# Kernel tuning notes

Hardware: AMD Instinct MI355X
Metric: run time of the kernel (lower is better)

Reference implementation:

```python
import math
import jax, jax.numpy as jnp
import numpy as np

E = 1024   # embed_dim
H = 16     # num_heads
DH = E // H
EPS = 1e-8

def round_ste(x):
    # straight-through round (matches brevitas STE behavior)
    return x + jax.lax.stop_gradient(jnp.round(x) - x)

def _scale(x, qmax):
    # dynamic per-tensor abs-max scale (stand-in for brevitas calibrated scale)
    return jnp.maximum(jnp.max(jnp.abs(x)) / qmax, EPS)

def fq(x, s, qmin, qmax):
    # fake-quantize: quantize to int grid, dequantize back to float
    return jnp.clip(round_ste(x / s), qmin, qmax) * s

def quant_linear(x, W, b):
    # Int8ActPerTensorFloat input, Int8WeightPerTensorFloat (narrow range) weight, Int32Bias
    s_x = _scale(x, 128.0)
    s_w = _scale(W, 127.0)
    xq = fq(x, s_x, -128, 127)
    wq = fq(W, s_w, -127, 127)
    y = xq @ wq.T
    if b is not None:
        s_b = s_x * s_w
        y = y + round_ste(b / s_b) * s_b
    return y

def setup_inputs() -> dict:
    k = jax.random.key(0)
    ks = jax.random.split(k, 7)
    S, B = 1024, 4
    return {
        "query": jax.random.normal(ks[0], (S, B, E), jnp.float32),
        "key": jax.random.normal(ks[1], (S, B, E), jnp.float32),
        "value": jax.random.normal(ks[2], (S, B, E), jnp.float32),
        "in_proj_weight": jax.random.normal(ks[3], (3 * E, E), jnp.float32) * 0.02,
        "in_proj_bias": jax.random.normal(ks[4], (3 * E,), jnp.float32) * 0.02,
        "out_proj_weight": jax.random.normal(ks[5], (E, E), jnp.float32) * 0.02,
        "out_proj_bias": jax.random.normal(ks[6], (E,), jnp.float32) * 0.02,
    }

def reference(query, key, value, in_proj_weight, in_proj_bias, out_proj_weight, out_proj_bias):
    S, B, _ = query.shape
    Wq, Wk, Wv = jnp.split(in_proj_weight, 3, axis=0)
    bq, bk, bv = jnp.split(in_proj_bias, 3)
    # quantized QKV projections (packed in_proj split per-input)
    q = quant_linear(query, Wq, bq)   # (S,B,E)
    k = quant_linear(key, Wk, bk)
    v = quant_linear(value, Wv, bv)

    def to_heads(x):  # (S,B,E) -> (B*H, S, DH)
        return x.reshape(S, B * H, DH).transpose(1, 0, 2)

    q = to_heads(q)
    k = to_heads(k)
    v = to_heads(v)

    # q_scaled quant (int8)
    q = q / math.sqrt(DH)
    q = fq(q, _scale(q, 128.0), -128, 127)
    # k_transposed quant (int8)
    kt = k.transpose(0, 2, 1)  # (B*H, DH, S)
    kt = fq(kt, _scale(kt, 128.0), -128, 127)

    attn = q @ kt                      # (B*H, S, S); softmax_input_quant=None -> identity
    attn = jax.nn.softmax(attn, axis=-1)
    # attn_output_weights quant (uint8)
    s_a = jnp.maximum(jnp.max(attn) / 255.0, EPS)
    attn = jnp.clip(round_ste(attn / s_a), 0, 255) * s_a
    # v quant (int8)
    v = fq(v, _scale(v, 128.0), -128, 127)

    out = attn @ v                     # (B*H, S, DH)
    out = out.transpose(1, 0, 2).reshape(S, B, E)
    out = quant_linear(out, out_proj_weight, out_proj_bias)
    return out
```

## Files before the change

### kernel.cpp

```cpp
#include <hip/hip_runtime.h>
#include <stdint.h>

typedef unsigned short u16;
typedef __attribute__((ext_vector_type(8))) short bf16x8;
typedef __attribute__((ext_vector_type(4))) float f32x4;

#define S_LEN 1024
#define BATCH 4
#define EMB   1024
#define NH    16
#define DHEAD 64
#define BHEAD 64
#define NTOK  4096
#define KDIM  1024
#define NDIM  1024
#define EPSF  1e-8f
#define LOG2E 1.4426950408889634f

#define MFMA16(a,b,c) __builtin_amdgcn_mfma_f32_16x16x32_bf16((a),(b),(c),0,0,0)

#define GLOAD16(g, l) __builtin_amdgcn_global_load_lds( \
    (const __attribute__((address_space(1))) void*)(g), \
    (__attribute__((address_space(3))) void*)(l), 16, 0, 0)

#define EXP2F(x) __builtin_amdgcn_exp2f(x)

__device__ __forceinline__ u16 f2bf(float f){
  return (u16)(__float_as_uint(f) >> 16);
}

__device__ __forceinline__ float wave_max(float v){
#pragma unroll
  for (int off = 32; off > 0; off >>= 1) v = fmaxf(v, __shfl_xor(v, off));
  return v;
}


__global__ void k_zero(float* sc){
  if (threadIdx.x < 16) sc[threadIdx.x] = 0.0f;
}

struct AQDesc { const float* x; u16* y; int n4; int slot; float qdiv; float lo; };
struct AQTable { AQDesc d[7]; };

__global__ __launch_bounds__(256) void k_absmax7(AQTable t, int* __restrict__ sci){
  const int bid = blockIdx.x;
  int seg, b0, nb;
  if (bid < 1536){ seg = bid >> 9; b0 = seg << 9; nb = 512; }
  else { seg = 3 + ((bid - 1536) >> 7); b0 = 1536 + ((seg - 3) << 7); nb = 128; }
  const AQDesc D = t.d[seg];
  float m = 0.0f;
  const float4* x4 = (const float4*)D.x;
  for (int i = (bid - b0)*256 + threadIdx.x; i < D.n4; i += nb*256){
    float4 v = x4[i];
    m = fmaxf(m, fmaxf(fmaxf(fabsf(v.x), fabsf(v.y)), fmaxf(fabsf(v.z), fabsf(v.w))));
  }
  m = wave_max(m);
  __shared__ float red[4];
  int lane = threadIdx.x & 63, w = threadIdx.x >> 6;
  if (lane == 0) red[w] = m;
  __syncthreads();
  if (threadIdx.x == 0){
    float mm = fmaxf(fmaxf(red[0], red[1]), fmaxf(red[2], red[3]));
    atomicMax(sci + D.slot, __float_as_int(mm));
  }
}

__global__ __launch_bounds__(256) void k_quant7(AQTable t, const float* __restrict__ sc){
  const int bid = blockIdx.x;
  int seg, b0, nb;
  if (bid < 1536){ seg = bid >> 9; b0 = seg << 9; nb = 512; }
  else { seg = 3 + ((bid - 1536) >> 7); b0 = 1536 + ((seg - 3) << 7); nb = 128; }
  const AQDesc D = t.d[seg];
  const float s = fmaxf(sc[D.slot] / D.qdiv, EPSF);
  const float lo = D.lo;
  const float4* x4 = (const float4*)D.x;
  for (int i = (bid - b0)*256 + threadIdx.x; i < D.n4; i += nb*256){
    float4 v = x4[i];
    union { u16 o[4]; uint2 u; } ou;
    float tt;
    tt = fminf(fmaxf(rintf(v.x / s), lo), 127.f); ou.o[0] = f2bf(tt);
    tt = fminf(fmaxf(rintf(v.y / s), lo), 127.f); ou.o[1] = f2bf(tt);
    tt = fminf(fmaxf(rintf(v.z / s), lo), 127.f); ou.o[2] = f2bf(tt);
    tt = fminf(fmaxf(rintf(v.w / s), lo), 127.f); ou.o[3] = f2bf(tt);
    ((uint2*)D.y)[i] = ou.u;
  }
}

__global__ __launch_bounds__(256) void k_quant(const float* __restrict__ x,
    u16* __restrict__ y, int n4, const float* __restrict__ sc, int slot){
  const float s = fmaxf(sc[slot] / 128.0f, EPSF);
  const float4* x4 = (const float4*)x;
  for (int i = blockIdx.x*256 + threadIdx.x; i < n4; i += gridDim.x*256){
    float4 v = x4[i];
    union { u16 o[4]; uint2 u; } ou;
    float tt;
    tt = fminf(fmaxf(rintf(v.x / s), -128.f), 127.f); ou.o[0] = f2bf(tt);
    tt = fminf(fmaxf(rintf(v.y / s), -128.f), 127.f); ou.o[1] = f2bf(tt);
    tt = fminf(fmaxf(rintf(v.z / s), -128.f), 127.f); ou.o[2] = f2bf(tt);
    tt = fminf(fmaxf(rintf(v.w / s), -128.f), 127.f); ou.o[3] = f2bf(tt);
    ((uint2*)y)[i] = ou.u;
  }
}

__device__ __forceinline__ void gemm_body(const u16* __restrict__ A,
    const u16* __restrict__ W, const float* __restrict__ bias,
    float* __restrict__ out, float s_b, int rowBase, int colBase,
    int* __restrict__ amax_out, u16 (*As)[32], u16 (*Bs)[32], float* red){
  const int tid = threadIdx.x;
  const int wid = tid >> 6, lane = tid & 63;
  const int wm = wid >> 2, wn = wid & 3;
  const int rr = lane & 15, kk = (lane >> 4) * 8;
  const int sr = tid >> 2, scb = (tid & 3) * 8;
  const u16* Arow = &A[(size_t)(rowBase + sr)*KDIM + scb];
  const u16* Wrow = &W[(size_t)(colBase + sr)*KDIM + scb];
  f32x4 c[4][2] = {};
  for (int k0 = 0; k0 < KDIM; k0 += 32){
    __syncthreads();
    GLOAD16(Arow + k0, &As[wid*16][0]);
    GLOAD16(Wrow + k0, &Bs[wid*16][0]);
    __syncthreads();
    bf16x8 af[4], bfr[2];
#pragma unroll
    for (int i = 0; i < 4; i++) af[i] = *(const bf16x8*)&As[wm*64 + i*16 + rr][kk];
#pragma unroll
    for (int j = 0; j < 2; j++) bfr[j] = *(const bf16x8*)&Bs[wn*32 + j*16 + rr][kk];
#pragma unroll
    for (int i = 0; i < 4; i++)
#pragma unroll
      for (int j = 0; j < 2; j++)
        c[i][j] = MFMA16(af[i], bfr[j], c[i][j]);
  }
  float lmax = 0.0f;
  const int r0 = (lane >> 4) * 4, ccol = lane & 15;
#pragma unroll
  for (int j = 0; j < 2; j++){
    int col = colBase + wn*32 + j*16 + ccol;
    float rb = rintf(bias[col] / s_b);
#pragma unroll
    for (int i = 0; i < 4; i++){
      int rowb = rowBase + wm*64 + i*16 + r0;
#pragma unroll
      for (int rI = 0; rI < 4; rI++){
        float y = s_b * (c[i][j][rI] + rb);
        out[(size_t)(rowb + rI)*NDIM + col] = y;
        lmax = fmaxf(lmax, fabsf(y));
      }
    }
  }
  lmax = wave_max(lmax);
  if (lane == 0) red[wid] = lmax;
  __syncthreads();
  if (tid == 0){
    float mm = red[0];
#pragma unroll
    for (int i2 = 1; i2 < 8; i2++) mm = fmaxf(mm, red[i2]);
    atomicMax(amax_out, __float_as_int(mm));
  }
}

__global__ __launch_bounds__(512) void k_gemm3(const u16* __restrict__ Xall,
    const u16* __restrict__ Wall, const float* __restrict__ ball,
    float* __restrict__ Yall, const float* __restrict__ sc, int* __restrict__ sci){
  __shared__ u16 As[128][32];
  __shared__ u16 Bs[128][32];
  __shared__ float red[8];
  const int orig = blockIdx.x;
  const int xcd = orig & 7, sl = orig >> 3;
  const int seg = sl >> 5;
  const int t2 = xcd*32 + (sl & 31);
  const int by = t2 >> 3, bx = t2 & 7;
  const float s_x = fmaxf(sc[seg] / 128.0f, EPSF);
  const float s_w = fmaxf(sc[3 + seg] / 127.0f, EPSF);
  gemm_body(Xall + (size_t)seg*NTOK*KDIM, Wall + (size_t)seg*KDIM*NDIM,
            ball + seg*1024, Yall + (size_t)seg*NTOK*NDIM, s_x*s_w,
            by*128, bx*128, sci + 7 + seg, As, Bs, red);
}

__global__ __launch_bounds__(512) void k_gemm1(const u16* __restrict__ A,
    const u16* __restrict__ W, const float* __restrict__ bias,
    float* __restrict__ out, const float* __restrict__ sc,
    int sx_slot, int sw_slot, int* __restrict__ amax_out){
  __shared__ u16 As[128][32];
  __shared__ u16 Bs[128][32];
  __shared__ float red[8];
  const int orig = blockIdx.x;
  const int t2 = (orig & 7)*32 + (orig >> 3);
  const int by = t2 >> 3, bx = t2 & 7;
  const float s_x = fmaxf(sc[sx_slot] / 128.0f, EPSF);
  const float s_w = fmaxf(sc[sw_slot] / 127.0f, EPSF);
  gemm_body(A, W, bias, out, s_x*s_w, by*128, bx*128, amax_out, As, Bs, red);
}

__global__ __launch_bounds__(256) void k_quant_heads(const float* __restrict__ qf,
    const float* __restrict__ kf, const float* __restrict__ vf,
    u16* __restrict__ qh, u16* __restrict__ kh, u16* __restrict__ vt,
    const float* __restrict__ sc){
  const float s_q = fmaxf((sc[7]*0.125f)/128.0f, EPSF);
  const float s_k = fmaxf(sc[8]/128.0f, EPSF);
  const float s_v = fmaxf(sc[9]/128.0f, EPSF);
  __shared__ u16 tile[64][80];
  const int bx = blockIdx.x;
  const int st = bx & 15, hh = (bx >> 4) & 15, b = bx >> 8;
  const int t = threadIdx.x;
  const int sl = t >> 2, dc = (t & 3) * 16;
  const size_t row = (size_t)(st*64 + sl)*BATCH + b;
  const size_t ibase = row*EMB + hh*DHEAD + dc;
  const int bh = b*NH + hh;
  float vq[16], vk[16], vv[16];
#pragma unroll
  for (int i = 0; i < 4; i++){
    *(float4*)&vq[i*4] = *(const float4*)&qf[ibase + i*4];
    *(float4*)&vk[i*4] = *(const float4*)&kf[ibase + i*4];
    *(float4*)&vv[i*4] = *(const float4*)&vf[ibase + i*4];
  }
  alignas(16) u16 oq[16], ok[16];
#pragma unroll
  for (int i = 0; i < 16; i++){
    float tq = fminf(fmaxf(rintf((vq[i]*0.125f)/s_q), -128.f), 127.f);
    float tk = fminf(fmaxf(rintf(vk[i]/s_k), -128.f), 127.f);
    float tv = fminf(fmaxf(rintf(vv[i]/s_v), -128.f), 127.f);
    oq[i] = f2bf(tq); ok[i] = f2bf(tk);
    tile[dc + i][sl] = f2bf(tv);
  }
  const size_t qoff = ((size_t)bh*S_LEN + st*64 + sl)*DHEAD + dc;
  *(bf16x8*)&qh[qoff]     = *(const bf16x8*)&oq[0];
  *(bf16x8*)&qh[qoff + 8] = *(const bf16x8*)&oq[8];
  *(bf16x8*)&kh[qoff]     = *(const bf16x8*)&ok[0];
  *(bf16x8*)&kh[qoff + 8] = *(const bf16x8*)&ok[8];
  __syncthreads();
  const int d = t >> 2, sc4 = (t & 3) * 16;
  alignas(16) u16 ov[16];
#pragma unroll
  for (int i = 0; i < 16; i++) ov[i] = tile[d][sc4 + i];
  const size_t voff = ((size_t)bh*DHEAD + d)*S_LEN + st*64 + sc4;
  *(bf16x8*)&vt[voff]     = *(const bf16x8*)&ov[0];
  *(bf16x8*)&vt[voff + 8] = *(const bf16x8*)&ov[8];
}

__global__ __launch_bounds__(256) void k_attn1(const u16* __restrict__ qh,
    const u16* __restrict__ kh, float* __restrict__ mrow, float* __restrict__ lrow,
    const float* __restrict__ sc, int* __restrict__ sci){
  __shared__ u16 Ks[64][64];
  __shared__ float red2[4];
  const int orig = blockIdx.x;
  const int tile = (orig & 7) * 128 + (orig >> 3);
  const int bhead = tile >> 4, q0 = (tile & 15) * 64;
  const int tid = threadIdx.x, w = tid >> 6, lane = tid & 63;
  const int rr = lane & 15, g = lane >> 4, kk = g * 8;
  const int lr3 = lane >> 3, lc = lane & 7;
  const float s_q = fmaxf((sc[7]*0.125f)/128.0f, EPSF);
  const float s_k = fmaxf(sc[8]/128.0f, EPSF);
  const float s_qk = s_q * s_k;
  const u16* qbase = qh + ((size_t)bhead*S_LEN + q0 + w*16)*DHEAD;
  const u16* kbase = kh + (size_t)bhead*S_LEN*DHEAD;
  bf16x8 a0 = *(const bf16x8*)&qbase[rr*DHEAD + kk];
  bf16x8 a1 = *(const bf16x8*)&qbase[rr*DHEAD + 32 + kk];
  float m[4] = {-1e30f, -1e30f, -1e30f, -1e30f};
  float l[4] = {0.f, 0.f, 0.f, 0.f};
  for (int cch = 0; cch < 16; cch++){
    const int n0 = cch * 64;
    __syncthreads();
#pragma unroll
    for (int i = 0; i < 2; i++){
      int r = w*16 + i*8 + lr3;
      GLOAD16(&kbase[(size_t)(n0 + r)*DHEAD + ((lc ^ (r & 7)) << 3)], &Ks[w*16 + i*8][0]);
    }
    __syncthreads();
    float sv[4][4];
#pragma unroll
    for (int nt = 0; nt < 4; nt++){
      int row = nt*16 + rr;
      bf16x8 b0 = *(const bf16x8*)((const u16*)Ks + row*64 + (((g    ) ^ (row & 7)) << 3));
      bf16x8 b1 = *(const bf16x8*)((const u16*)Ks + row*64 + (((4 + g) ^ (row & 7)) << 3));
      f32x4 acc = {};
      acc = MFMA16(a0, b0, acc);
      acc = MFMA16(a1, b1, acc);
#pragma unroll
      for (int r = 0; r < 4; r++) sv[nt][r] = acc[r]*s_qk;
    }
#pragma unroll
    for (int r = 0; r < 4; r++){
      float cm = fmaxf(fmaxf(sv[0][r], sv[1][r]), fmaxf(sv[2][r], sv[3][r]));
      float mn = fmaxf(m[r], cm);
      l[r] *= EXP2F((m[r] - mn)*LOG2E);
      m[r] = mn;
#pragma unroll
      for (int nt = 0; nt < 4; nt++)
        l[r] += EXP2F((sv[nt][r] - m[r])*LOG2E);
    }
  }
#pragma unroll
  for (int off = 1; off < 16; off <<= 1){
#pragma unroll
    for (int r = 0; r < 4; r++){
      float mo = __shfl_xor(m[r], off), lo = __shfl_xor(l[r], off);
      float mn = fmaxf(m[r], mo);
      l[r] = l[r]*EXP2F((m[r] - mn)*LOG2E) + lo*EXP2F((mo - mn)*LOG2E);
      m[r] = mn;
    }
  }
  if (rr == 0){
    int rowb = q0 + w*16 + g*4;
#pragma unroll
    for (int r = 0; r < 4; r++){
      mrow[(size_t)bhead*S_LEN + rowb + r] = m[r];
      lrow[(size_t)bhead*S_LEN + rowb + r] = l[r];
    }
  }
  float im = 0.0f;
#pragma unroll
  for (int r = 0; r < 4; r++) im = fmaxf(im, 1.0f / l[r]);
  im = wave_max(im);
  if (lane == 0) red2[w] = im;
  __syncthreads();
  if (tid == 0){
    float mm = fmaxf(fmaxf(red2[0], red2[1]), fmaxf(red2[2], red2[3]));
    atomicMax(sci + 13, __float_as_int(mm));
  }
}

__global__ void k_sa_final(float* sc, const int* sci){
  if (threadIdx.x == 0)
    sc[11] = fmaxf(__int_as_float(sci[13]) / 255.0f, EPSF);
}

__global__ __launch_bounds__(256) void k_attn2(const u16* __restrict__ qh,
    const u16* __restrict__ kh, const u16* __restrict__ vt,
    const float* __restrict__ mrow, const float* __restrict__ lrow,
    float* __restrict__ aout, const float* __restrict__ sc, int* __restrict__ amax_out){
  __shared__ u16 Ks[64][64];
  __shared__ u16 Vs[64][64];
  __shared__ u16 P[4][16][72];
  __shared__ float red[4];
  const int orig = blockIdx.x;
  const int tile = (orig & 7) * 128 + (orig >> 3);
  const int bhead = tile >> 4, q0 = (tile & 15) * 64;
  const int tid = threadIdx.x, w = tid >> 6, lane = tid & 63;
  const int rr = lane & 15, g = lane >> 4, kk = g * 8;
  const int lr3 = lane >> 3, lc = lane & 7;
  const float s_q = fmaxf((sc[7]*0.125f)/128.0f, EPSF);
  const float s_k = fmaxf(sc[8]/128.0f, EPSF);
  const float s_qk = s_q * s_k;
  const float s_v = fmaxf(sc[9]/128.0f, EPSF);
  const float s_a = sc[11];
  const float fac = s_a * s_v;
  const u16* qbase = qh + ((size_t)bhead*S_LEN + q0 + w*16)*DHEAD;
  const u16* kbase = kh + (size_t)bhead*S_LEN*DHEAD;
  const u16* vbase = vt + (size_t)bhead*DHEAD*S_LEN;
  bf16x8 a0 = *(const bf16x8*)&qbase[rr*DHEAD + kk];
  bf16x8 a1 = *(const bf16x8*)&qbase[rr*DHEAD + 32 + kk];
  float mr[4], inv[4];
  {
    int rowb = q0 + w*16 + g*4;
#pragma unroll
    for (int r = 0; r < 4; r++){
      mr[r]  = mrow[(size_t)bhead*S_LEN + rowb + r];
      inv[r] = 1.0f / (lrow[(size_t)bhead*S_LEN + rowb + r] * s_a);
    }
  }
  f32x4 cpv[4] = {};
  for (int cch = 0; cch < 16; cch++){
    const int n0 = cch * 64;
    __syncthreads();
#pragma unroll
    for (int i = 0; i < 2; i++){
      int r = w*16 + i*8 + lr3;
      GLOAD16(&kbase[(size_t)(n0 + r)*DHEAD + ((lc ^ (r & 7)) << 3)], &Ks[w*16 + i*8][0]);
      int d = w*16 + i*8 + lr3;
      GLOAD16(&vbase[(size_t)d*S_LEN + n0 + ((lc ^ (d & 7)) << 3)], &Vs[w*16 + i*8][0]);
    }
    __syncthreads();
#pragma unroll
    for (int nt = 0; nt < 4; nt++){
      int row = nt*16 + rr;
      bf16x8 b0 = *(const bf16x8*)((const u16*)Ks + row*64 + (((g    ) ^ (row & 7)) << 3));
      bf16x8 b1 = *(const bf16x8*)((const u16*)Ks + row*64 + (((4 + g) ^ (row & 7)) << 3));
      f32x4 acc = {};
      acc = MFMA16(a0, b0, acc);
      acc = MFMA16(a1, b1, acc);
#pragma unroll
      for (int r = 0; r < 4; r++){
        float e  = EXP2F((acc[r]*s_qk - mr[r])*LOG2E);
        float pq = fminf(rintf(e * inv[r]), 255.0f);
        P[w][g*4 + r][nt*16 + rr] = f2bf(pq);
      }
    }
    bf16x8 pa0 = *(const bf16x8*)&P[w][rr][kk];
    bf16x8 pa1 = *(const bf16x8*)&P[w][rr][32 + kk];
#pragma unroll
    for (int f = 0; f < 4; f++){
      int row = f*16 + rr;
      bf16x8 v0 = *(const bf16x8*)((const u16*)Vs + row*64 + (((g    ) ^ (row & 7)) << 3));
      bf16x8 v1 = *(const bf16x8*)((const u16*)Vs + row*64 + (((4 + g) ^ (row & 7)) << 3));
      cpv[f] = MFMA16(pa0, v0, cpv[f]);
      cpv[f] = MFMA16(pa1, v1, cpv[f]);
    }
  }
  const int b = bhead >> 4, hh = bhead & 15;
  float lmax = 0.0f;
#pragma unroll
  for (int f = 0; f < 4; f++){
    int d = f*16 + rr;
#pragma unroll
    for (int r = 0; r < 4; r++){
      int srow = q0 + w*16 + g*4 + r;
      float y = fac * cpv[f][r];
      aout[(size_t)(srow*BATCH + b)*EMB + hh*DHEAD + d] = y;
      lmax = fmaxf(lmax, fabsf(y));
    }
  }
  lmax = wave_max(lmax);
  __syncthreads();
  if (lane == 0) red[w] = lmax;
  __syncthreads();
  if (tid == 0){
    float mm = fmaxf(fmaxf(red[0], red[1]), fmaxf(red[2], red[3]));
    atomicMax(amax_out, __float_as_int(mm));
  }
}

extern "C" void kernel_launch(void* const* d_in, const int* in_sizes, int n_in,
                              void* d_out, int out_size, void* d_ws, size_t ws_size,
                              hipStream_t stream){
  const float* query = (const float*)d_in[0];
  const float* key   = (const float*)d_in[1];
  const float* value = (const float*)d_in[2];
  const float* inW   = (const float*)d_in[3];
  const float* inB   = (const float*)d_in[4];
  const float* outW  = (const float*)d_in[5];
  const float* outB  = (const float*)d_in[6];
  float* out = (float*)d_out;

  char* ws = (char*)d_ws;
  float* sc  = (float*)ws;
  int*   sci = (int*)ws;
  u16* WQQ = (u16*)(ws + 256);
  u16* WKQ = WQQ + 1024*1024;
  u16* WVQ = WKQ + 1024*1024;
  u16* WOQ = WVQ + 1024*1024;
  u16* XQ  = WOQ + 1024*1024;
  u16* XK  = XQ + NTOK*1024;
  u16* XV  = XK + NTOK*1024;
  float* QF = (float*)(XV + NTOK*1024);
  float* KF = QF + NTOK*1024;
  float* VF = KF + NTOK*1024;
  float* MROW = VF + NTOK*1024;
  float* LROW = MROW + BHEAD*S_LEN;
  u16* QH = XQ;  u16* KH = XK;  u16* VT = XV;
  float* AOUT = QF;
  u16* AOQ = (u16*)KF;

  AQTable tab;
  tab.d[0] = { query,             XQ,  NTOK*1024/4, 0, 128.f, -128.f };
  tab.d[1] = { key,               XK,  NTOK*1024/4, 1, 128.f, -128.f };
  tab.d[2] = { value,             XV,  NTOK*1024/4, 2, 128.f, -128.f };
  tab.d[3] = { inW,               WQQ, 1024*1024/4, 3, 127.f, -127.f };
  tab.d[4] = { inW + 1024*1024,   WKQ, 1024*1024/4, 4, 127.f, -127.f };
  tab.d[5] = { inW + 2*1024*1024, WVQ, 1024*1024/4, 5, 127.f, -127.f };
  tab.d[6] = { outW,              WOQ, 1024*1024/4, 6, 127.f, -127.f };

  k_zero<<<1, 64, 0, stream>>>(sc);
  k_absmax7<<<2048, 256, 0, stream>>>(tab, sci);
  k_quant7<<<2048, 256, 0, stream>>>(tab, sc);
  k_gemm3<<<768, 512, 0, stream>>>(XQ, WQQ, inB, QF, sc, sci);
  k_quant_heads<<<1024, 256, 0, stream>>>(QF, KF, VF, QH, KH, VT, sc);
  k_attn1<<<1024, 256, 0, stream>>>(QH, KH, MROW, LROW, sc, sci);
  k_sa_final<<<1, 64, 0, stream>>>(sc, sci);
  k_attn2<<<1024, 256, 0, stream>>>(QH, KH, VT, MROW, LROW, AOUT, sc, sci + 10);
  k_quant<<<1024, 256, 0, stream>>>(AOUT, AOQ, NTOK*1024/4, sc, 10);
  k_gemm1<<<256, 512, 0, stream>>>(AOQ, WOQ, outB, out, sc, 10, 6, sci + 12);
}
```

Measured before the change: 215.0 us.

## Double-buffer LDS tiles in GEMM and attention kernels, swizzle, drop sa_final

Adds double-buffered LDS tiles to the GEMM and both attention kernels. The load of the next K-step or chunk is issued before the current one is consumed, and one barrier per iteration replaces two. It also XOR-swizzles the GEMM A/B tiles and the P scratch buffer to cut LDS bank conflicts. It removes the separate k_sa_final launch by computing s_a inside k_attn2, and replaces block reductions with per-wave atomics. The cost is double the LDS use and more atomics, which may lower occupancy.

```diff
diff --git a/kernel.cpp b/kernel.cpp
--- a/kernel.cpp
+++ b/kernel.cpp
@@ -106,30 +106,48 @@
 __device__ __forceinline__ void gemm_body(const u16* __restrict__ A,
     const u16* __restrict__ W, const float* __restrict__ bias,
     float* __restrict__ out, float s_b, int rowBase, int colBase,
-    int* __restrict__ amax_out, u16 (*As)[32], u16 (*Bs)[32], float* red){
+    int* __restrict__ amax_out, u16 (*As)[128][32], u16 (*Bs)[128][32], float* red){
   const int tid = threadIdx.x;
   const int wid = tid >> 6, lane = tid & 63;
   const int wm = wid >> 2, wn = wid & 3;
-  const int rr = lane & 15, kk = (lane >> 4) * 8;
-  const int sr = tid >> 2, scb = (tid & 3) * 8;
-  const u16* Arow = &A[(size_t)(rowBase + sr)*KDIM + scb];
-  const u16* Wrow = &W[(size_t)(colBase + sr)*KDIM + scb];
+  const int rr = lane & 15, g = lane >> 4, kk = g * 8;
+  const int sr = tid >> 2, sc4 = tid & 3;
+  const int scol = (sc4 ^ ((sr >> 1) & 3)) * 8;
+  const u16* Arow = &A[(size_t)(rowBase + sr)*KDIM + scol];
+  const u16* Wrow = &W[(size_t)(colBase + sr)*KDIM + scol];
   f32x4 c[4][2] = {};
+  int aoff[4], boff[2];
+#pragma unroll
+  for (int i = 0; i < 4; i++){
+    int row = wm*64 + i*16 + rr;
+    aoff[i] = row*32 + ((g ^ ((row >> 1) & 3)) << 3);
+  }
+#pragma unroll
+  for (int j = 0; j < 2; j++){
+    int row = wn*32 + j*16 + rr;
+    boff[j] = row*32 + ((g ^ ((row >> 1) & 3)) << 3);
+  }
+  GLOAD16(Arow, &As[0][sr][sc4*8]);
+  GLOAD16(Wrow, &Bs[0][sr][sc4*8]);
+  __syncthreads();
+  int cur = 0;
   for (int k0 = 0; k0 < KDIM; k0 += 32){
-    __syncthreads();
-    GLOAD16(Arow + k0, &As[wid*16][0]);
-    GLOAD16(Wrow + k0, &Bs[wid*16][0]);
-    __syncthreads();
+    if (k0 + 32 < KDIM){
+      GLOAD16(Arow + k0 + 32, &As[cur^1][sr][sc4*8]);
+      GLOAD16(Wrow + k0 + 32, &Bs[cur^1][sr][sc4*8]);
+    }
     bf16x8 af[4], bfr[2];
 #pragma unroll
-    for (int i = 0; i < 4; i++) af[i] = *(const bf16x8*)&As[wm*64 + i*16 + rr][kk];
-#pragma unroll
-    for (int j = 0; j < 2; j++) bfr[j] = *(const bf16x8*)&Bs[wn*32 + j*16 + rr][kk];
+    for (int i = 0; i < 4; i++) af[i]  = *(const bf16x8*)((const u16*)As[cur] + aoff[i]);
+#pragma unroll
+    for (int j = 0; j < 2; j++) bfr[j] = *(const bf16x8*)((const u16*)Bs[cur] + boff[j]);
 #pragma unroll
     for (int i = 0; i < 4; i++)
 #pragma unroll
       for (int j = 0; j < 2; j++)
         c[i][j] = MFMA16(af[i], bfr[j], c[i][j]);
+    __syncthreads();
+    cur ^= 1;
   }
   float lmax = 0.0f;
   const int r0 = (lane >> 4) * 4, ccol = lane & 15;
@@ -162,8 +180,8 @@
 __global__ __launch_bounds__(512) void k_gemm3(const u16* __restrict__ Xall,
     const u16* __restrict__ Wall, const float* __restrict__ ball,
     float* __restrict__ Yall, const float* __restrict__ sc, int* __restrict__ sci){
-  __shared__ u16 As[128][32];
-  __shared__ u16 Bs[128][32];
+  __shared__ u16 As[2][128][32];
+  __shared__ u16 Bs[2][128][32];
   __shared__ float red[8];
   const int orig = blockIdx.x;
   const int xcd = orig & 7, sl = orig >> 3;
@@ -181,8 +199,8 @@
     const u16* __restrict__ W, const float* __restrict__ bias,
     float* __restrict__ out, const float* __restrict__ sc,
     int sx_slot, int sw_slot, int* __restrict__ amax_out){
-  __shared__ u16 As[128][32];
-  __shared__ u16 Bs[128][32];
+  __shared__ u16 As[2][128][32];
+  __shared__ u16 Bs[2][128][32];
   __shared__ float red[8];
   const int orig = blockIdx.x;
   const int t2 = (orig & 7)*32 + (orig >> 3);
@@ -241,8 +259,7 @@
 __global__ __launch_bounds__(256) void k_attn1(const u16* __restrict__ qh,
     const u16* __restrict__ kh, float* __restrict__ mrow, float* __restrict__ lrow,
     const float* __restrict__ sc, int* __restrict__ sci){
-  __shared__ u16 Ks[64][64];
-  __shared__ float red2[4];
+  __shared__ u16 Ks[2][64][64];
   const int orig = blockIdx.x;
   const int tile = (orig & 7) * 128 + (orig >> 3);
   const int bhead = tile >> 4, q0 = (tile & 15) * 64;
@@ -256,23 +273,26 @@
   const u16* kbase = kh + (size_t)bhead*S_LEN*DHEAD;
   bf16x8 a0 = *(const bf16x8*)&qbase[rr*DHEAD + kk];
   bf16x8 a1 = *(const bf16x8*)&qbase[rr*DHEAD + 32 + kk];
+  const int sr0 = w*16 + lr3, sr1 = w*16 + 8 + lr3;
+  const int sco0 = (lc ^ (sr0 & 7)) << 3, sco1 = (lc ^ (sr1 & 7)) << 3;
+  GLOAD16(&kbase[(size_t)sr0*DHEAD + sco0], &Ks[0][w*16][0]);
+  GLOAD16(&kbase[(size_t)sr1*DHEAD + sco1], &Ks[0][w*16 + 8][0]);
+  __syncthreads();
+  int cur = 0;
   float m[4] = {-1e30f, -1e30f, -1e30f, -1e30f};
   float l[4] = {0.f, 0.f, 0.f, 0.f};
   for (int cch = 0; cch < 16; cch++){
-    const int n0 = cch * 64;
-    __syncthreads();
-#pragma unroll
-    for (int i = 0; i < 2; i++){
-      int r = w*16 + i*8 + lr3;
-      GLOAD16(&kbase[(size_t)(n0 + r)*DHEAD + ((lc ^ (r & 7)) << 3)], &Ks[w*16 + i*8][0]);
-    }
-    __syncthreads();
+    if (cch < 15){
+      const int n0 = (cch + 1) * 64;
+      GLOAD16(&kbase[(size_t)(n0 + sr0)*DHEAD + sco0], &Ks[cur^1][w*16][0]);
+      GLOAD16(&kbase[(size_t)(n0 + sr1)*DHEAD + sco1], &Ks[cur^1][w*16 + 8][0]);
+    }
     float sv[4][4];
 #pragma unroll
     for (int nt = 0; nt < 4; nt++){
       int row = nt*16 + rr;
-      bf16x8 b0 = *(const bf16x8*)((const u16*)Ks + row*64 + (((g    ) ^ (row & 7)) << 3));
-      bf16x8 b1 = *(const bf16x8*)((const u16*)Ks + row*64 + (((4 + g) ^ (row & 7)) << 3));
+      bf16x8 b0 = *(const bf16x8*)((const u16*)Ks[cur] + row*64 + (((g    ) ^ (row & 7)) << 3));
+      bf16x8 b1 = *(const bf16x8*)((const u16*)Ks[cur] + row*64 + (((4 + g) ^ (row & 7)) << 3));
       f32x4 acc = {};
       acc = MFMA16(a0, b0, acc);
       acc = MFMA16(a1, b1, acc);
@@ -289,6 +309,8 @@
       for (int nt = 0; nt < 4; nt++)
         l[r] += EXP2F((sv[nt][r] - m[r])*LOG2E);
     }
+    __syncthreads();
+    cur ^= 1;
   }
 #pragma unroll
   for (int off = 1; off < 16; off <<= 1){
@@ -312,27 +334,17 @@
 #pragma unroll
   for (int r = 0; r < 4; r++) im = fmaxf(im, 1.0f / l[r]);
   im = wave_max(im);
-  if (lane == 0) red2[w] = im;
-  __syncthreads();
-  if (tid == 0){
-    float mm = fmaxf(fmaxf(red2[0], red2[1]), fmaxf(red2[2], red2[3]));
-    atomicMax(sci + 13, __float_as_int(mm));
-  }
-}
-
-__global__ void k_sa_final(float* sc, const int* sci){
-  if (threadIdx.x == 0)
-    sc[11] = fmaxf(__int_as_float(sci[13]) / 255.0f, EPSF);
+  if (lane == 0) atomicMax(sci + 13, __float_as_int(im));
 }
 
 __global__ __launch_bounds__(256) void k_attn2(const u16* __restrict__ qh,
     const u16* __restrict__ kh, const u16* __restrict__ vt,
     const float* __restrict__ mrow, const float* __restrict__ lrow,
-    float* __restrict__ aout, const float* __restrict__ sc, int* __restrict__ amax_out){
-  __shared__ u16 Ks[64][64];
-  __shared__ u16 Vs[64][64];
-  __shared__ u16 P[4][16][72];
-  __shared__ float red[4];
+    float* __restrict__ aout, const float* __restrict__ sc,
+    const int* __restrict__ sci, int* __restrict__ amax_out){
+  __shared__ u16 Ks[2][64][64];
+  __shared__ u16 Vs[2][64][64];
+  __shared__ u16 P[4][16][64];
   const int orig = blockIdx.x;
   const int tile = (orig & 7) * 128 + (orig >> 3);
   const int bhead = tile >> 4, q0 = (tile & 15) * 64;
@@ -343,7 +355,7 @@
   const float s_k = fmaxf(sc[8]/128.0f, EPSF);
   const float s_qk = s_q * s_k;
   const float s_v = fmaxf(sc[9]/128.0f, EPSF);
-  const float s_a = sc[11];
+  const float s_a = fmaxf(__int_as_float(sci[13]) / 255.0f, EPSF);
   const float fac = s_a * s_v;
   const u16* qbase = qh + ((size_t)bhead*S_LEN + q0 + w*16)*DHEAD;
   const u16* kbase = kh + (size_t)bhead*S_LEN*DHEAD;
@@ -359,23 +371,30 @@
       inv[r] = 1.0f / (lrow[(size_t)bhead*S_LEN + rowb + r] * s_a);
     }
   }
+  const int sr0 = w*16 + lr3, sr1 = w*16 + 8 + lr3;
+  const int sco0 = (lc ^ (sr0 & 7)) << 3, sco1 = (lc ^ (sr1 & 7)) << 3;
+  GLOAD16(&kbase[(size_t)sr0*DHEAD + sco0], &Ks[0][w*16][0]);
+  GLOAD16(&kbase[(size_t)sr1*DHEAD + sco1], &Ks[0][w*16 + 8][0]);
+  GLOAD16(&vbase[(size_t)sr0*S_LEN + sco0], &Vs[0][w*16][0]);
+  GLOAD16(&vbase[(size_t)sr1*S_LEN + sco1], &Vs[0][w*16 + 8][0]);
+  __syncthreads();
+  int cur = 0;
   f32x4 cpv[4] = {};
+  const int poff0 = rr*64 + (((g    ) ^ (rr & 7)) << 3);
+  const int poff1 = rr*64 + (((4 + g) ^ (rr & 7)) << 3);
   for (int cch = 0; cch < 16; cch++){
-    const int n0 = cch * 64;
-    __syncthreads();
-#pragma unroll
-    for (int i = 0; i < 2; i++){
-      int r = w*16 + i*8 + lr3;
-      GLOAD16(&kbase[(size_t)(n0 + r)*DHEAD + ((lc ^ (r & 7)) << 3)], &Ks[w*16 + i*8][0]);
-      int d = w*16 + i*8 + lr3;
-      GLOAD16(&vbase[(size_t)d*S_LEN + n0 + ((lc ^ (d & 7)) << 3)], &Vs[w*16 + i*8][0]);
-    }
-    __syncthreads();
+    if (cch < 15){
+      const int n0 = (cch + 1) * 64;
+      GLOAD16(&kbase[(size_t)(n0 + sr0)*DHEAD + sco0], &Ks[cur^1][w*16][0]);
+      GLOAD16(&kbase[(size_t)(n0 + sr1)*DHEAD + sco1], &Ks[cur^1][w*16 + 8][0]);
+      GLOAD16(&vbase[(size_t)sr0*S_LEN + n0 + sco0], &Vs[cur^1][w*16][0]);
+      GLOAD16(&vbase[(size_t)sr1*S_LEN + n0 + sco1], &Vs[cur^1][w*16 + 8][0]);
+    }
 #pragma unroll
     for (int nt = 0; nt < 4; nt++){
       int row = nt*16 + rr;
-      bf16x8 b0 = *(const bf16x8*)((const u16*)Ks + row*64 + (((g    ) ^ (row & 7)) << 3));
-      bf16x8 b1 = *(const bf16x8*)((const u16*)Ks + row*64 + (((4 + g) ^ (row & 7)) << 3));
+      bf16x8 b0 = *(const bf16x8*)((const u16*)Ks[cur] + row*64 + (((g    ) ^ (row & 7)) << 3));
+      bf16x8 b1 = *(const bf16x8*)((const u16*)Ks[cur] + row*64 + (((4 + g) ^ (row & 7)) << 3));
       f32x4 acc = {};
       acc = MFMA16(a0, b0, acc);
       acc = MFMA16(a1, b1, acc);
@@ -383,19 +402,24 @@
       for (int r = 0; r < 4; r++){
         float e  = EXP2F((acc[r]*s_qk - mr[r])*LOG2E);
         float pq = fminf(rintf(e * inv[r]), 255.0f);
-        P[w][g*4 + r][nt*16 + rr] = f2bf(pq);
+        int prow = g*4 + r;
+        int pcol = nt*16 + rr;
+        int pch  = ((pcol >> 3) ^ (prow & 7)) << 3;
+        P[w][prow][pch | (pcol & 7)] = f2bf(pq);
       }
     }
-    bf16x8 pa0 = *(const bf16x8*)&P[w][rr][kk];
-    bf16x8 pa1 = *(const bf16x8*)&P[w][rr][32 + kk];
+    bf16x8 pa0 = *(const bf16x8*)((const u16*)P[w] + poff0);
+    bf16x8 pa1 = *(const bf16x8*)((const u16*)P[w] + poff1);
 #pragma unroll
     for (int f = 0; f < 4; f++){
       int row = f*16 + rr;
-      bf16x8 v0 = *(const bf16x8*)((const u16*)Vs + row*64 + (((g    ) ^ (row & 7)) << 3));
-      bf16x8 v1 = *(const bf16x8*)((const u16*)Vs + row*64 + (((4 + g) ^ (row & 7)) << 3));
+      bf16x8 v0 = *(const bf16x8*)((const u16*)Vs[cur] + row*64 + (((g    ) ^ (row & 7)) << 3));
+      bf16x8 v1 = *(const bf16x8*)((const u16*)Vs[cur] + row*64 + (((4 + g) ^ (row & 7)) << 3));
       cpv[f] = MFMA16(pa0, v0, cpv[f]);
       cpv[f] = MFMA16(pa1, v1, cpv[f]);
     }
+    __syncthreads();
+    cur ^= 1;
   }
   const int b = bhead >> 4, hh = bhead & 15;
   float lmax = 0.0f;
@@ -411,13 +435,7 @@
     }
   }
   lmax = wave_max(lmax);
-  __syncthreads();
-  if (lane == 0) red[w] = lmax;
-  __syncthreads();
-  if (tid == 0){
-    float mm = fmaxf(fmaxf(red[0], red[1]), fmaxf(red[2], red[3]));
-    atomicMax(amax_out, __float_as_int(mm));
-  }
+  if (lane == 0) atomicMax(amax_out, __float_as_int(lmax));
 }
 
 extern "C" void kernel_launch(void* const* d_in, const int* in_sizes, int n_in,
@@ -466,8 +484,7 @@
   k_gemm3<<<768, 512, 0, stream>>>(XQ, WQQ, inB, QF, sc, sci);
   k_quant_heads<<<1024, 256, 0, stream>>>(QF, KF, VF, QH, KH, VT, sc);
   k_attn1<<<1024, 256, 0, stream>>>(QH, KH, MROW, LROW, sc, sci);
-  k_sa_final<<<1, 64, 0, stream>>>(sc, sci);
-  k_attn2<<<1024, 256, 0, stream>>>(QH, KH, VT, MROW, LROW, AOUT, sc, sci + 10);
+  k_attn2<<<1024, 256, 0, stream>>>(QH, KH, VT, MROW, LROW, AOUT, sc, sci, sci + 10);
   k_quant<<<1024, 256, 0, stream>>>(AOUT, AOQ, NTOK*1024/4, sc, 10);
   k_gemm1<<<256, 512, 0, stream>>>(AOQ, WOQ, outB, out, sc, 10, 6, sci + 12);
 }
```

New measurement: 288.0 us. 1.34x slower.

## Double attention query tile per block, swizzle GEMM LDS, drop scale-finalize kernel

Applied to the files above, without the earlier changes.

The attention kernels now use 512-thread blocks covering 128 query rows, so each K/V chunk loaded into LDS is reused by twice as many waves and half as many blocks are launched. Per-wave atomics replace the block-level LDS reduction, and the separate one-thread kernel that finalized the attention scale is removed; attn2 computes that scale inline. The GEMM body applies an XOR swizzle to its LDS tile layout to avoid bank conflicts on fragment reads. In exchange, more atomics hit global memory and fewer blocks are available for latency hiding.

```diff
diff --git a/kernel.cpp b/kernel.cpp
--- a/kernel.cpp
+++ b/kernel.cpp
@@ -110,11 +110,23 @@
   const int tid = threadIdx.x;
   const int wid = tid >> 6, lane = tid & 63;
   const int wm = wid >> 2, wn = wid & 3;
-  const int rr = lane & 15, kk = (lane >> 4) * 8;
-  const int sr = tid >> 2, scb = (tid & 3) * 8;
-  const u16* Arow = &A[(size_t)(rowBase + sr)*KDIM + scb];
-  const u16* Wrow = &W[(size_t)(colBase + sr)*KDIM + scb];
+  const int rr = lane & 15, g = lane >> 4, kk = g * 8;
+  const int sr = tid >> 2, sc4 = tid & 3;
+  const int scol = (sc4 ^ ((sr >> 1) & 3)) * 8;
+  const u16* Arow = &A[(size_t)(rowBase + sr)*KDIM + scol];
+  const u16* Wrow = &W[(size_t)(colBase + sr)*KDIM + scol];
   f32x4 c[4][2] = {};
+  int aoff[4], boff[2];
+#pragma unroll
+  for (int i = 0; i < 4; i++){
+    int row = wm*64 + i*16 + rr;
+    aoff[i] = row*32 + ((g ^ ((row >> 1) & 3)) << 3);
+  }
+#pragma unroll
+  for (int j = 0; j < 2; j++){
+    int row = wn*32 + j*16 + rr;
+    boff[j] = row*32 + ((g ^ ((row >> 1) & 3)) << 3);
+  }
   for (int k0 = 0; k0 < KDIM; k0 += 32){
     __syncthreads();
     GLOAD16(Arow + k0, &As[wid*16][0]);
@@ -122,9 +134,9 @@
     __syncthreads();
     bf16x8 af[4], bfr[2];
 #pragma unroll
-    for (int i = 0; i < 4; i++) af[i] = *(const bf16x8*)&As[wm*64 + i*16 + rr][kk];
-#pragma unroll
-    for (int j = 0; j < 2; j++) bfr[j] = *(const bf16x8*)&Bs[wn*32 + j*16 + rr][kk];
+    for (int i = 0; i < 4; i++) af[i]  = *(const bf16x8*)((const u16*)As + aoff[i]);
+#pragma unroll
+    for (int j = 0; j < 2; j++) bfr[j] = *(const bf16x8*)((const u16*)Bs + boff[j]);
 #pragma unroll
     for (int i = 0; i < 4; i++)
 #pragma unroll
@@ -238,17 +250,15 @@
   *(bf16x8*)&vt[voff + 8] = *(const bf16x8*)&ov[8];
 }
 
-__global__ __launch_bounds__(256) void k_attn1(const u16* __restrict__ qh,
+__global__ __launch_bounds__(512) void k_attn1(const u16* __restrict__ qh,
     const u16* __restrict__ kh, float* __restrict__ mrow, float* __restrict__ lrow,
     const float* __restrict__ sc, int* __restrict__ sci){
   __shared__ u16 Ks[64][64];
-  __shared__ float red2[4];
   const int orig = blockIdx.x;
-  const int tile = (orig & 7) * 128 + (orig >> 3);
-  const int bhead = tile >> 4, q0 = (tile & 15) * 64;
+  const int tile = (orig & 7) * 64 + (orig >> 3);
+  const int bhead = tile >> 3, q0 = (tile & 7) * 128;
   const int tid = threadIdx.x, w = tid >> 6, lane = tid & 63;
   const int rr = lane & 15, g = lane >> 4, kk = g * 8;
-  const int lr3 = lane >> 3, lc = lane & 7;
   const float s_q = fmaxf((sc[7]*0.125f)/128.0f, EPSF);
   const float s_k = fmaxf(sc[8]/128.0f, EPSF);
   const float s_qk = s_q * s_k;
@@ -256,16 +266,14 @@
   const u16* kbase = kh + (size_t)bhead*S_LEN*DHEAD;
   bf16x8 a0 = *(const bf16x8*)&qbase[rr*DHEAD + kk];
   bf16x8 a1 = *(const bf16x8*)&qbase[rr*DHEAD + 32 + kk];
+  const int rowc = w*8 + (lane >> 3);
+  const int scol = ((lane & 7) ^ (rowc & 7)) << 3;
   float m[4] = {-1e30f, -1e30f, -1e30f, -1e30f};
   float l[4] = {0.f, 0.f, 0.f, 0.f};
   for (int cch = 0; cch < 16; cch++){
     const int n0 = cch * 64;
     __syncthreads();
-#pragma unroll
-    for (int i = 0; i < 2; i++){
-      int r = w*16 + i*8 + lr3;
-      GLOAD16(&kbase[(size_t)(n0 + r)*DHEAD + ((lc ^ (r & 7)) << 3)], &Ks[w*16 + i*8][0]);
-    }
+    GLOAD16(&kbase[(size_t)(n0 + rowc)*DHEAD + scol], &Ks[w*8][0]);
     __syncthreads();
     float sv[4][4];
 #pragma unroll
@@ -312,38 +320,27 @@
 #pragma unroll
   for (int r = 0; r < 4; r++) im = fmaxf(im, 1.0f / l[r]);
   im = wave_max(im);
-  if (lane == 0) red2[w] = im;
-  __syncthreads();
-  if (tid == 0){
-    float mm = fmaxf(fmaxf(red2[0], red2[1]), fmaxf(red2[2], red2[3]));
-    atomicMax(sci + 13, __float_as_int(mm));
-  }
-}
-
-__global__ void k_sa_final(float* sc, const int* sci){
-  if (threadIdx.x == 0)
-    sc[11] = fmaxf(__int_as_float(sci[13]) / 255.0f, EPSF);
-}
-
-__global__ __launch_bounds__(256) void k_attn2(const u16* __restrict__ qh,
+  if (lane == 0) atomicMax(sci + 13, __float_as_int(im));
+}
+
+__global__ __launch_bounds__(512) void k_attn2(const u16* __restrict__ qh,
     const u16* __restrict__ kh, const u16* __restrict__ vt,
     const float* __restrict__ mrow, const float* __restrict__ lrow,
-    float* __restrict__ aout, const float* __restrict__ sc, int* __restrict__ amax_out){
+    float* __restrict__ aout, const float* __restrict__ sc,
+    const int* __restrict__ sci, int* __restrict__ amax_out){
   __shared__ u16 Ks[64][64];
   __shared__ u16 Vs[64][64];
-  __shared__ u16 P[4][16][72];
-  __shared__ float red[4];
+  __shared__ u16 P[8][16][72];
   const int orig = blockIdx.x;
-  const int tile = (orig & 7) * 128 + (orig >> 3);
-  const int bhead = tile >> 4, q0 = (tile & 15) * 64;
+  const int tile = (orig & 7) * 64 + (orig >> 3);
+  const int bhead = tile >> 3, q0 = (tile & 7) * 128;
   const int tid = threadIdx.x, w = tid >> 6, lane = tid & 63;
   const int rr = lane & 15, g = lane >> 4, kk = g * 8;
-  const int lr3 = lane >> 3, lc = lane & 7;
   const float s_q = fmaxf((sc[7]*0.125f)/128.0f, EPSF);
   const float s_k = fmaxf(sc[8]/128.0f, EPSF);
   const float s_qk = s_q * s_k;
   const float s_v = fmaxf(sc[9]/128.0f, EPSF);
-  const float s_a = sc[11];
+  const float s_a = fmaxf(__int_as_float(sci[13]) / 255.0f, EPSF);
   const float fac = s_a * s_v;
   const u16* qbase = qh + ((size_t)bhead*S_LEN + q0 + w*16)*DHEAD;
   const u16* kbase = kh + (size_t)bhead*S_LEN*DHEAD;
@@ -359,17 +356,14 @@
       inv[r] = 1.0f / (lrow[(size_t)bhead*S_LEN + rowb + r] * s_a);
     }
   }
+  const int rowc = w*8 + (lane >> 3);
+  const int scol = ((lane & 7) ^ (rowc & 7)) << 3;
   f32x4 cpv[4] = {};
   for (int cch = 0; cch < 16; cch++){
     const int n0 = cch * 64;
     __syncthreads();
-#pragma unroll
-    for (int i = 0; i < 2; i++){
-      int r = w*16 + i*8 + lr3;
-      GLOAD16(&kbase[(size_t)(n0 + r)*DHEAD + ((lc ^ (r & 7)) << 3)], &Ks[w*16 + i*8][0]);
-      int d = w*16 + i*8 + lr3;
-      GLOAD16(&vbase[(size_t)d*S_LEN + n0 + ((lc ^ (d & 7)) << 3)], &Vs[w*16 + i*8][0]);
-    }
+    GLOAD16(&kbase[(size_t)(n0 + rowc)*DHEAD + scol], &Ks[w*8][0]);
+    GLOAD16(&vbase[(size_t)rowc*S_LEN + n0 + scol], &Vs[w*8][0]);
     __syncthreads();
 #pragma unroll
     for (int nt = 0; nt < 4; nt++){
@@ -411,13 +405,7 @@
     }
   }
   lmax = wave_max(lmax);
-  __syncthreads();
-  if (lane == 0) red[w] = lmax;
-  __syncthreads();
-  if (tid == 0){
-    float mm = fmaxf(fmaxf(red[0], red[1]), fmaxf(red[2], red[3]));
-    atomicMax(amax_out, __float_as_int(mm));
-  }
+  if (lane == 0) atomicMax(amax_out, __float_as_int(lmax));
 }
 
 extern "C" void kernel_launch(void* const* d_in, const int* in_sizes, int n_in,
@@ -465,9 +453,8 @@
   k_quant7<<<2048, 256, 0, stream>>>(tab, sc);
   k_gemm3<<<768, 512, 0, stream>>>(XQ, WQQ, inB, QF, sc, sci);
   k_quant_heads<<<1024, 256, 0, stream>>>(QF, KF, VF, QH, KH, VT, sc);
-  k_attn1<<<1024, 256, 0, stream>>>(QH, KH, MROW, LROW, sc, sci);
-  k_sa_final<<<1, 64, 0, stream>>>(sc, sci);
-  k_attn2<<<1024, 256, 0, stream>>>(QH, KH, VT, MROW, LROW, AOUT, sc, sci + 10);
+  k_attn1<<<512, 512, 0, stream>>>(QH, KH, MROW, LROW, sc, sci);
+  k_attn2<<<512, 512, 0, stream>>>(QH, KH, VT, MROW, LROW, AOUT, sc, sci, sci + 10);
   k_quant<<<1024, 256, 0, stream>>>(AOUT, AOQ, NTOK*1024/4, sc, 10);
   k_gemm1<<<256, 512, 0, stream>>>(AOQ, WOQ, outB, out, sc, 10, 6, sci + 12);
 }
```

Measured after the change: 282.9 us. 31.6% more time.

## Double GEMM K-tile to 64 with XOR-swizzled LDS, drop sa_final launch

Applied to the files above, without the earlier changes.

The shared GEMM body now stages 64-wide K slices per iteration instead of 32, which halves the number of barrier pairs per K loop. LDS rows are XOR-swizzled so the 128-byte rows do not cause bank conflicts on fragment reads. The separate single-thread kernel that computed the attention-weight scale is removed, and k_attn2 derives that scale itself from the integer amax. k_attn2's block reduction is also replaced by a per-wave atomicMax, which removes two barriers at the cost of more atomics.

```diff
diff --git a/kernel.cpp b/kernel.cpp
--- a/kernel.cpp
+++ b/kernel.cpp
@@ -106,30 +106,53 @@
 __device__ __forceinline__ void gemm_body(const u16* __restrict__ A,
     const u16* __restrict__ W, const float* __restrict__ bias,
     float* __restrict__ out, float s_b, int rowBase, int colBase,
-    int* __restrict__ amax_out, u16 (*As)[32], u16 (*Bs)[32], float* red){
+    int* __restrict__ amax_out, u16 (*As)[64], u16 (*Bs)[64], float* red){
   const int tid = threadIdx.x;
   const int wid = tid >> 6, lane = tid & 63;
   const int wm = wid >> 2, wn = wid & 3;
-  const int rr = lane & 15, kk = (lane >> 4) * 8;
-  const int sr = tid >> 2, scb = (tid & 3) * 8;
-  const u16* Arow = &A[(size_t)(rowBase + sr)*KDIM + scb];
-  const u16* Wrow = &W[(size_t)(colBase + sr)*KDIM + scb];
+  const int rr = lane & 15, g = lane >> 4;
+  const int srow = wid*8 + (lane >> 3);
+  const int sco  = ((lane & 7) ^ (lane >> 3)) << 3;
+  const u16* Arow0 = &A[(size_t)(rowBase + srow)*KDIM + sco];
+  const u16* Arow1 = &A[(size_t)(rowBase + 64 + srow)*KDIM + sco];
+  const u16* Wrow0 = &W[(size_t)(colBase + srow)*KDIM + sco];
+  const u16* Wrow1 = &W[(size_t)(colBase + 64 + srow)*KDIM + sco];
   f32x4 c[4][2] = {};
-  for (int k0 = 0; k0 < KDIM; k0 += 32){
-    __syncthreads();
-    GLOAD16(Arow + k0, &As[wid*16][0]);
-    GLOAD16(Wrow + k0, &Bs[wid*16][0]);
-    __syncthreads();
-    bf16x8 af[4], bfr[2];
-#pragma unroll
-    for (int i = 0; i < 4; i++) af[i] = *(const bf16x8*)&As[wm*64 + i*16 + rr][kk];
-#pragma unroll
-    for (int j = 0; j < 2; j++) bfr[j] = *(const bf16x8*)&Bs[wn*32 + j*16 + rr][kk];
-#pragma unroll
-    for (int i = 0; i < 4; i++)
-#pragma unroll
-      for (int j = 0; j < 2; j++)
-        c[i][j] = MFMA16(af[i], bfr[j], c[i][j]);
+  int aoff[4][2], boff[2][2];
+#pragma unroll
+  for (int i = 0; i < 4; i++){
+    int row = wm*64 + i*16 + rr;
+#pragma unroll
+    for (int h = 0; h < 2; h++)
+      aoff[i][h] = row*64 + (((h*4 + g) ^ (row & 7)) << 3);
+  }
+#pragma unroll
+  for (int j = 0; j < 2; j++){
+    int row = wn*32 + j*16 + rr;
+#pragma unroll
+    for (int h = 0; h < 2; h++)
+      boff[j][h] = row*64 + (((h*4 + g) ^ (row & 7)) << 3);
+  }
+  for (int k0 = 0; k0 < KDIM; k0 += 64){
+    __syncthreads();
+    GLOAD16(Arow0 + k0, &As[wid*8][0]);
+    GLOAD16(Arow1 + k0, &As[64 + wid*8][0]);
+    GLOAD16(Wrow0 + k0, &Bs[wid*8][0]);
+    GLOAD16(Wrow1 + k0, &Bs[64 + wid*8][0]);
+    __syncthreads();
+#pragma unroll
+    for (int h = 0; h < 2; h++){
+      bf16x8 af[4], bfr[2];
+#pragma unroll
+      for (int i = 0; i < 4; i++) af[i]  = *(const bf16x8*)((const u16*)As + aoff[i][h]);
+#pragma unroll
+      for (int j = 0; j < 2; j++) bfr[j] = *(const bf16x8*)((const u16*)Bs + boff[j][h]);
+#pragma unroll
+      for (int i = 0; i < 4; i++)
+#pragma unroll
+        for (int j = 0; j < 2; j++)
+          c[i][j] = MFMA16(af[i], bfr[j], c[i][j]);
+    }
   }
   float lmax = 0.0f;
   const int r0 = (lane >> 4) * 4, ccol = lane & 15;
@@ -162,8 +185,8 @@
 __global__ __launch_bounds__(512) void k_gemm3(const u16* __restrict__ Xall,
     const u16* __restrict__ Wall, const float* __restrict__ ball,
     float* __restrict__ Yall, const float* __restrict__ sc, int* __restrict__ sci){
-  __shared__ u16 As[128][32];
-  __shared__ u16 Bs[128][32];
+  __shared__ u16 As[128][64];
+  __shared__ u16 Bs[128][64];
   __shared__ float red[8];
   const int orig = blockIdx.x;
   const int xcd = orig & 7, sl = orig >> 3;
@@ -181,8 +204,8 @@
     const u16* __restrict__ W, const float* __restrict__ bias,
     float* __restrict__ out, const float* __restrict__ sc,
     int sx_slot, int sw_slot, int* __restrict__ amax_out){
-  __shared__ u16 As[128][32];
-  __shared__ u16 Bs[128][32];
+  __shared__ u16 As[128][64];
+  __shared__ u16 Bs[128][64];
   __shared__ float red[8];
   const int orig = blockIdx.x;
   const int t2 = (orig & 7)*32 + (orig >> 3);
@@ -320,19 +343,14 @@
   }
 }
 
-__global__ void k_sa_final(float* sc, const int* sci){
-  if (threadIdx.x == 0)
-    sc[11] = fmaxf(__int_as_float(sci[13]) / 255.0f, EPSF);
-}
-
 __global__ __launch_bounds__(256) void k_attn2(const u16* __restrict__ qh,
     const u16* __restrict__ kh, const u16* __restrict__ vt,
     const float* __restrict__ mrow, const float* __restrict__ lrow,
-    float* __restrict__ aout, const float* __restrict__ sc, int* __restrict__ amax_out){
+    float* __restrict__ aout, const float* __restrict__ sc,
+    const int* __restrict__ sci, int* __restrict__ amax_out){
   __shared__ u16 Ks[64][64];
   __shared__ u16 Vs[64][64];
   __shared__ u16 P[4][16][72];
-  __shared__ float red[4];
   const int orig = blockIdx.x;
   const int tile = (orig & 7) * 128 + (orig >> 3);
   const int bhead = tile >> 4, q0 = (tile & 15) * 64;
@@ -343,7 +361,7 @@
   const float s_k = fmaxf(sc[8]/128.0f, EPSF);
   const float s_qk = s_q * s_k;
   const float s_v = fmaxf(sc[9]/128.0f, EPSF);
-  const float s_a = sc[11];
+  const float s_a = fmaxf(__int_as_float(sci[13]) / 255.0f, EPSF);
   const float fac = s_a * s_v;
   const u16* qbase = qh + ((size_t)bhead*S_LEN + q0 + w*16)*DHEAD;
   const u16* kbase = kh + (size_t)bhead*S_LEN*DHEAD;
@@ -411,13 +429,7 @@
     }
   }
   lmax = wave_max(lmax);
-  __syncthreads();
-  if (lane == 0) red[w] = lmax;
-  __syncthreads();
-  if (tid == 0){
-    float mm = fmaxf(fmaxf(red[0], red[1]), fmaxf(red[2], red[3]));
-    atomicMax(amax_out, __float_as_int(mm));
-  }
+  if (lane == 0) atomicMax(amax_out, __float_as_int(lmax));
 }
 
 extern "C" void kernel_launch(void* const* d_in, const int* in_sizes, int n_in,
@@ -466,8 +478,7 @@
   k_gemm3<<<768, 512, 0, stream>>>(XQ, WQQ, inB, QF, sc, sci);
   k_quant_heads<<<1024, 256, 0, stream>>>(QF, KF, VF, QH, KH, VT, sc);
   k_attn1<<<1024, 256, 0, stream>>>(QH, KH, MROW, LROW, sc, sci);
-  k_sa_final<<<1, 64, 0, stream>>>(sc, sci);
-  k_attn2<<<1024, 256, 0, stream>>>(QH, KH, VT, MROW, LROW, AOUT, sc, sci + 10);
+  k_attn2<<<1024, 256, 0, stream>>>(QH, KH, VT, MROW, LROW, AOUT, sc, sci, sci + 10);
   k_quant<<<1024, 256, 0, stream>>>(AOUT, AOQ, NTOK*1024/4, sc, 10);
   k_gemm1<<<256, 512, 0, stream>>>(AOQ, WOQ, outB, out, sc, 10, 6, sci + 12);
 }
```

New measurement: 244.3 us. +13.6%, slower.
